# Kernel optimization log

Measured on AMD Instinct MI355X. Metric: run time of the kernel, lower is better.

## Reference

```python
import jax, jax.numpy as jnp
import numpy as np

DIM = 192
SHIFT = 3
PAD = SHIFT // 2  # 1
EPS = 1e-5


def conv1x1(x, w, b):
    # 1x1x1 Conv3d == channel matmul. x: (B,C,D,H,W), w: (O,C), b: (O,)
    return jnp.einsum('bcdhw,oc->bodhw', x, w) + b[None, :, None, None, None]


def group_norm1(x, w, b):
    # GroupNorm(1, C): normalize over (C,D,H,W) per sample, per-channel affine.
    mu = x.mean(axis=(1, 2, 3, 4), keepdims=True)
    var = x.var(axis=(1, 2, 3, 4), keepdims=True)
    xn = (x - mu) * jax.lax.rsqrt(var + EPS)
    return xn * w[None, :, None, None, None] + b[None, :, None, None, None]


def axial_shift(x, axis):
    # reflect-pad all 3 spatial dims, roll channel-chunks along `axis`, crop back.
    R = x.shape[-1]
    xp = jnp.pad(x, ((0, 0), (0, 0), (PAD, PAD), (PAD, PAD), (PAD, PAD)), mode='reflect')
    chunks = jnp.split(xp, SHIFT, axis=1)
    rolled = [jnp.roll(c, s, axis=axis) for c, s in zip(chunks, range(-PAD, PAD + 1))]
    xc = jnp.concatenate(rolled, axis=1)
    return xc[:, :, PAD:PAD + R, PAD:PAD + R, PAD:PAD + R]


def setup_inputs() -> dict:
    key = jax.random.key(0)
    ks = jax.random.split(key, 16)
    B, C, R = 8, DIM, 32
    x = jax.random.normal(ks[0], (B, C, R, R, R), dtype=jnp.float32)
    wmat = lambda k: jax.random.normal(k, (C, C), dtype=jnp.float32) * 0.05
    vec = lambda k: jax.random.normal(k, (C,), dtype=jnp.float32) * 0.05
    return {
        'x': x,
        'w1': wmat(ks[1]), 'b1': vec(ks[2]),
        'n1w': jnp.ones((C,), jnp.float32), 'n1b': jnp.zeros((C,), jnp.float32),
        'w21': wmat(ks[3]), 'b21': vec(ks[4]),
        'w22': wmat(ks[5]), 'b22': vec(ks[6]),
        'w23': wmat(ks[7]), 'b23': vec(ks[8]),
        'n2w': jnp.ones((C,), jnp.float32), 'n2b': jnp.zeros((C,), jnp.float32),
        'w3': wmat(ks[9]), 'b3': vec(ks[10]),
    }


def reference(x, w1, b1, n1w, n1b, w21, b21, w22, b22, w23, b23, n2w, n2b, w3, b3):
    h = conv1x1(x, w1, b1)
    h = group_norm1(h, n1w, n1b)
    h = jax.nn.gelu(h, approximate=False)
    h = axial_shift(h, axis=3)
    h = conv1x1(h, w22, b22)
    h = axial_shift(h, axis=2)
    h = conv1x1(h, w21, b21)
    h = axial_shift(h, axis=4)
    h = conv1x1(h, w23, b23)
    h = jax.nn.gelu(h, approximate=False)
    h = group_norm1(h, n2w, n2b)
    h = conv1x1(h, w3, b3)
    return h
```

## Files before the change

### kernel.cpp

```cpp
#include <hip/hip_runtime.h>
#include <math.h>

#define NCH 192
#define NB 8
#define SPAT 32768
#define TILE_M 64
#define TILES_PER_B (SPAT / TILE_M)
#define NWG (NB * TILES_PER_B)
#define NELEM_PER_B ((size_t)NCH * SPAT)

typedef short s16x8 __attribute__((ext_vector_type(8)));
typedef float f32x4 __attribute__((ext_vector_type(4)));

__device__ __forceinline__ float bf2f(unsigned short h) {
  return __uint_as_float(((unsigned)h) << 16);
}
__device__ __forceinline__ unsigned short f2bf(float f) {
  unsigned u = __float_as_uint(f);
  u += 0x7FFF + ((u >> 16) & 1);
  return (unsigned short)(u >> 16);
}

__device__ __forceinline__ float erf_fast(float x) {
  float ax = fabsf(x);
  float t = 1.0f / fmaf(0.3275911f, ax, 1.0f);
  float p = t * fmaf(t, fmaf(t, fmaf(t, fmaf(t, 1.061405429f, -1.453152027f),
                                     1.421413741f), -0.284496736f), 0.254829592f);
  float r = 1.0f - p * __expf(-ax * ax);
  return copysignf(r, x);
}
__device__ __forceinline__ float gelu_exact(float x) {
  return 0.5f * x * (1.0f + erf_fast(x * 0.70710678118654752f));
}

template <int AX>
__device__ __forceinline__ int shift_src(int p, int s) {
  if (AX == 0) return p;
  const int SH = (AX == 4) ? 0 : (AX == 3) ? 5 : 10;
  int i = (p >> SH) & 31;
  int j = i - s;
  j = (j < 0) ? 1 : j;
  j = (j > 31) ? 30 : j;
  return p + ((j - i) << SH);
}

__device__ __forceinline__ int lds_off(int c, int p, int inner_byte) {
  return (c * 64 + p) * 128 + (inner_byte ^ ((p & 7) << 4));
}

template <int AX, int EPI, int OUTF, int INF, int PERB, int FUSE>
__global__ __launch_bounds__(256, 4)
void gemm_pass(const void* __restrict__ inv,
               const unsigned short* __restrict__ wmat,
               const float* __restrict__ bias,
               void* __restrict__ outv,
               float* __restrict__ partials,
               const float* __restrict__ AC) {
  __shared__ __align__(16) char lds[3 * 64 * 128];
  __shared__ float acs[2 * NCH];
  __shared__ float red[4][2];

  int wg = blockIdx.x;
  int b = wg / TILES_PER_B;
  int p0 = (wg % TILES_PER_B) * TILE_M;
  int tid = threadIdx.x;
  int wave = tid >> 6;
  int lane = tid & 63;
  int col = lane & 15;
  int kg = lane >> 4;

  const unsigned short* wbase = wmat + (PERB ? (size_t)b * NCH * NCH : 0);
  const float* bbase = bias + (PERB ? b * NCH : 0);
  const char* inbytes = (const char*)inv;
  const float* xin = (const float*)inv;

  if (FUSE) {
    for (int i = tid; i < 2 * NCH; i += 256) acs[i] = AC[b * 2 * NCH + i];
    __syncthreads();
  }

  if (INF == 1) {
    int c3 = tid >> 6;
    int p = tid & 63;
    if (c3 < 3) {
      const float* src = xin + (size_t)b * NELEM_PER_B +
                         (size_t)(c3 * 64) * SPAT + (p0 + p);
#pragma unroll
      for (int j = 0; j < 8; ++j) {
        s16x8 v;
#pragma unroll
        for (int u = 0; u < 8; ++u)
          v[u] = (short)f2bf(src[(size_t)(8 * j + u) * SPAT]);
        *(s16x8*)(lds + lds_off(c3, p, j * 16)) = v;
      }
    }
  } else {
#pragma unroll
    for (int j = 0; j < 6; ++j) {
      unsigned g = j * 256 + tid;
      int p = (int)(g / 24u);
      int r24 = (int)(g - 24u * (unsigned)p);
      int c = r24 >> 3;
      int ps = shift_src<AX>(p0 + p, c - 1);
      s16x8 v = *(const s16x8*)(inbytes + ((size_t)b * SPAT + ps) * 384 + r24 * 16);
      if (FUSE) {
        int ch0 = r24 * 8;
#pragma unroll
        for (int u = 0; u < 8; ++u) {
          float f = bf2f((unsigned short)v[u]);
          f = fmaf(f, acs[ch0 + u], acs[NCH + ch0 + u]);
          f = gelu_exact(f);
          v[u] = (short)f2bf(f);
        }
      }
      *(s16x8*)(lds + lds_off(c, p, (r24 & 7) * 16)) = v;
    }
  }
  __syncthreads();

  f32x4 acc[3][4] = {};
#pragma unroll
  for (int ks = 0; ks < 6; ++ks) {
    int k0 = ks * 32 + kg * 8;
    s16x8 af[3];
#pragma unroll
    for (int r = 0; r < 3; ++r) {
      int row = wave * 48 + r * 16 + col;
      af[r] = *(const s16x8*)(wbase + row * NCH + k0);
    }
    int c = k0 >> 6, u = k0 & 63;
    s16x8 bf[4];
#pragma unroll
    for (int m = 0; m < 4; ++m)
      bf[m] = *(const s16x8*)(lds + lds_off(c, m * 16 + col, 2 * u));
#pragma unroll
    for (int r = 0; r < 3; ++r)
#pragma unroll
      for (int m = 0; m < 4; ++m)
        acc[r][m] = __builtin_amdgcn_mfma_f32_16x16x32_bf16(af[r], bf[m], acc[r][m], 0, 0, 0);
  }

  float ssum = 0.f, ssq = 0.f;
  float* outf = (float*)outv;
  if (OUTF == 0) __syncthreads();
#pragma unroll
  for (int r = 0; r < 3; ++r) {
    int rowb = wave * 48 + r * 16 + kg * 4;
    f32x4 bs = *(const f32x4*)(bbase + rowb);
#pragma unroll
    for (int m = 0; m < 4; ++m) {
      int p = m * 16 + col;
      float v[4];
#pragma unroll
      for (int j = 0; j < 4; ++j) {
        float t = acc[r][m][j] + bs[j];
        if (EPI == 2) t = gelu_exact(t);
        if (EPI >= 1) { ssum += t; ssq = fmaf(t, t, ssq); }
        v[j] = t;
      }
      if (OUTF == 0) {
        uint2 pk;
        pk.x = (unsigned)f2bf(v[0]) | ((unsigned)f2bf(v[1]) << 16);
        pk.y = (unsigned)f2bf(v[2]) | ((unsigned)f2bf(v[3]) << 16);
        *(uint2*)(lds + lds_off(rowb >> 6, p, 2 * (rowb & 63))) = pk;
      } else {
#pragma unroll
        for (int j = 0; j < 4; ++j)
          outf[((size_t)b * NCH + rowb + j) * SPAT + p0 + p] = v[j];
      }
    }
  }

  if (OUTF == 0) {
    __syncthreads();
    char* outbytes = (char*)outv + ((size_t)b * SPAT + p0) * 384;
#pragma unroll
    for (int j = 0; j < 6; ++j) {
      unsigned g = j * 256 + tid;
      int p = (int)(g / 24u);
      int r24 = (int)(g - 24u * (unsigned)p);
      int c = r24 >> 3;
      s16x8 v = *(const s16x8*)(lds + lds_off(c, p, (r24 & 7) * 16));
      *(s16x8*)(outbytes + g * 16) = v;
    }
  }

  if (EPI >= 1) {
#pragma unroll
    for (int off = 1; off < 64; off <<= 1) {
      ssum += __shfl_xor(ssum, off, 64);
      ssq += __shfl_xor(ssq, off, 64);
    }
    if (lane == 0) { red[wave][0] = ssum; red[wave][1] = ssq; }
    __syncthreads();
    if (tid == 0) {
      partials[wg * 2]     = red[0][0] + red[1][0] + red[2][0] + red[3][0];
      partials[wg * 2 + 1] = red[0][1] + red[1][1] + red[2][1] + red[3][1];
    }
  }
}

__global__ void stats_finalize(const float* __restrict__ partials,
                               const float* __restrict__ nw,
                               const float* __restrict__ nb,
                               float* __restrict__ AC) {
  int b = blockIdx.x;
  int tid = threadIdx.x;
  __shared__ float s0[256], s1[256];
  float a = 0.f, c = 0.f;
  for (int i = tid; i < TILES_PER_B; i += 256) {
    a += partials[(b * TILES_PER_B + i) * 2];
    c += partials[(b * TILES_PER_B + i) * 2 + 1];
  }
  s0[tid] = a; s1[tid] = c;
  __syncthreads();
  for (int st = 128; st > 0; st >>= 1) {
    if (tid < st) { s0[tid] += s0[tid + st]; s1[tid] += s1[tid + st]; }
    __syncthreads();
  }
  float inv_n = 1.0f / (float)(NELEM_PER_B);
  float mu = s0[0] * inv_n;
  float var = s1[0] * inv_n - mu * mu;
  float rs = rsqrtf(var + 1e-5f);
  if (tid < NCH) {
    float A = rs * nw[tid];
    AC[b * 2 * NCH + tid] = A;
    AC[b * 2 * NCH + NCH + tid] = nb[tid] - mu * A;
  }
}

__global__ void prep_weights(const float* __restrict__ w1, const float* __restrict__ w21,
                             const float* __restrict__ w22, const float* __restrict__ w23,
                             unsigned short* __restrict__ wb) {
  int i = blockIdx.x * 256 + threadIdx.x;
  if (i >= 4 * NCH * NCH) return;
  int m = i / (NCH * NCH), r = i % (NCH * NCH);
  const float* src = (m == 0) ? w1 : (m == 1) ? w22 : (m == 2) ? w21 : w23;
  wb[i] = f2bf(src[r]);
}

__global__ void prep_w3(const float* __restrict__ w3, const float* __restrict__ b3,
                        const float* __restrict__ AC2,
                        unsigned short* __restrict__ w3e, float* __restrict__ b3e) {
  int b = blockIdx.x;
  int o = threadIdx.x;
  if (o >= NCH) return;
  const float* A = AC2 + b * 2 * NCH;
  const float* C = A + NCH;
  float s = b3[o];
  for (int c = 0; c < NCH; ++c) {
    float w = w3[o * NCH + c];
    w3e[((size_t)b * NCH + o) * NCH + c] = f2bf(w * A[c]);
    s = fmaf(w, C[c], s);
  }
  b3e[b * NCH + o] = s;
}

extern "C" void kernel_launch(void* const* d_in, const int* in_sizes, int n_in,
                              void* d_out, int out_size, void* d_ws, size_t ws_size,
                              hipStream_t stream) {
  const float* x   = (const float*)d_in[0];
  const float* w1  = (const float*)d_in[1];
  const float* b1  = (const float*)d_in[2];
  const float* n1w = (const float*)d_in[3];
  const float* n1b = (const float*)d_in[4];
  const float* w21 = (const float*)d_in[5];
  const float* b21 = (const float*)d_in[6];
  const float* w22 = (const float*)d_in[7];
  const float* b22 = (const float*)d_in[8];
  const float* w23 = (const float*)d_in[9];
  const float* b23 = (const float*)d_in[10];
  const float* n2w = (const float*)d_in[11];
  const float* n2b = (const float*)d_in[12];
  const float* w3  = (const float*)d_in[13];
  const float* b3  = (const float*)d_in[14];

  char* ws = (char*)d_ws;
  size_t off = 0;
  unsigned short* wb = (unsigned short*)(ws + off); off += (size_t)4 * NCH * NCH * 2;
  off = (off + 255) & ~(size_t)255;
  unsigned short* w3e = (unsigned short*)(ws + off); off += (size_t)NB * NCH * NCH * 2;
  off = (off + 255) & ~(size_t)255;
  float* b3e = (float*)(ws + off); off += NB * NCH * 4;
  float* AC1 = (float*)(ws + off); off += NB * 2 * NCH * 4;
  float* AC2 = (float*)(ws + off); off += NB * 2 * NCH * 4;
  float* part1 = (float*)(ws + off); off += NWG * 2 * 4;
  float* part2 = (float*)(ws + off); off += NWG * 2 * 4;
  off = (off + 255) & ~(size_t)255;
  unsigned short* R1 = (unsigned short*)(ws + off);
  unsigned short* R2 = (unsigned short*)d_out;

  prep_weights<<<(4 * NCH * NCH + 255) / 256, 256, 0, stream>>>(w1, w21, w22, w23, wb);

  gemm_pass<0, 1, 0, 1, 0, 0><<<NWG, 256, 0, stream>>>(x, wb + 0 * NCH * NCH, b1, R2, part1, nullptr);
  stats_finalize<<<NB, 256, 0, stream>>>(part1, n1w, n1b, AC1);
  gemm_pass<3, 0, 0, 0, 0, 1><<<NWG, 256, 0, stream>>>(R2, wb + 1 * NCH * NCH, b22, R1, nullptr, AC1);
  gemm_pass<2, 0, 0, 0, 0, 0><<<NWG, 256, 0, stream>>>(R1, wb + 2 * NCH * NCH, b21, R2, nullptr, nullptr);
  gemm_pass<4, 2, 0, 0, 0, 0><<<NWG, 256, 0, stream>>>(R2, wb + 3 * NCH * NCH, b23, R1, part2, nullptr);
  stats_finalize<<<NB, 256, 0, stream>>>(part2, n2w, n2b, AC2);
  prep_w3<<<NB, NCH, 0, stream>>>(w3, b3, AC2, w3e, b3e);
  gemm_pass<0, 0, 1, 0, 1, 0><<<NWG, 256, 0, stream>>>(R1, w3e, b3e, d_out, part2, nullptr);
}
```

Measured before the change: 388.4 us.

## Make GEMM passes persistent over 8 tiles with register prefetch and double-buffered LDS

Each workgroup now processes 8 consecutive 64-position tiles instead of one, shrinking the grid to 512 workgroups. The weight fragments are loaded into registers once per workgroup rather than once per tile. The next tile's global loads are issued into registers while the current tile is staged and multiplied, alternating between two LDS buffers. The first pass also reads fp32 input with vector loads, and the LDS swizzle is changed. The costs are higher register pressure (launch bounds lowered to 2 waves per SIMD), double the LDS footprint, and fewer workgroups, which may underfill the GPU.

```diff
diff --git a/kernel.cpp b/kernel.cpp
--- a/kernel.cpp
+++ b/kernel.cpp
@@ -5,8 +5,8 @@
 #define NB 8
 #define SPAT 32768
 #define TILE_M 64
-#define TILES_PER_B (SPAT / TILE_M)
-#define NWG (NB * TILES_PER_B)
+#define TPW 8
+#define NWG_P 512
 #define NELEM_PER_B ((size_t)NCH * SPAT)
 
 typedef short s16x8 __attribute__((ext_vector_type(8)));
@@ -44,25 +44,25 @@
   return p + ((j - i) << SH);
 }
 
-__device__ __forceinline__ int lds_off(int c, int p, int inner_byte) {
-  return (c * 64 + p) * 128 + (inner_byte ^ ((p & 7) << 4));
+__device__ __forceinline__ int lds_off(int c, int p, int u) {
+  return (c * 64 + p) * 128 + 16 * (((u >> 3) ^ (p & 7) ^ (p >> 3)) & 7) + 2 * (u & 7);
 }
 
 template <int AX, int EPI, int OUTF, int INF, int PERB, int FUSE>
-__global__ __launch_bounds__(256, 4)
+__global__ __launch_bounds__(256, 2)
 void gemm_pass(const void* __restrict__ inv,
                const unsigned short* __restrict__ wmat,
                const float* __restrict__ bias,
                void* __restrict__ outv,
                float* __restrict__ partials,
                const float* __restrict__ AC) {
-  __shared__ __align__(16) char lds[3 * 64 * 128];
+  __shared__ __align__(16) char lds[2][3 * 64 * 128];
   __shared__ float acs[2 * NCH];
   __shared__ float red[4][2];
 
   int wg = blockIdx.x;
-  int b = wg / TILES_PER_B;
-  int p0 = (wg % TILES_PER_B) * TILE_M;
+  int b = wg >> 6;
+  int ti0 = (wg & 63) * TPW;
   int tid = threadIdx.x;
   int wave = tid >> 6;
   int lane = tid & 63;
@@ -73,115 +73,150 @@
   const float* bbase = bias + (PERB ? b * NCH : 0);
   const char* inbytes = (const char*)inv;
   const float* xin = (const float*)inv;
-
-  if (FUSE) {
+  float* outf = (float*)outv;
+
+  s16x8 af[6][3];
+#pragma unroll
+  for (int ks = 0; ks < 6; ++ks)
+#pragma unroll
+    for (int r = 0; r < 3; ++r)
+      af[ks][r] = *(const s16x8*)(wbase + (wave * 48 + r * 16 + col) * NCH + ks * 32 + kg * 8);
+
+  if (FUSE)
     for (int i = tid; i < 2 * NCH; i += 256) acs[i] = AC[b * 2 * NCH + i];
+
+  s16x8 vr[6];
+  f32x4 xr[12];
+  {
+    int p0 = ti0 * 64;
+    if (INF == 1) {
+#pragma unroll
+      for (int j = 0; j < 12; ++j) {
+        int q = j * 256 + tid, ch = q >> 4, g = q & 15;
+        xr[j] = *(const f32x4*)(xin + (size_t)b * NELEM_PER_B + (size_t)ch * SPAT + p0 + 4 * g);
+      }
+    } else {
+#pragma unroll
+      for (int j = 0; j < 6; ++j) {
+        unsigned g = j * 256 + tid;
+        int p = (int)(g / 24u), r24 = (int)(g - 24u * (unsigned)p);
+        int ps = shift_src<AX>(p0 + p, (r24 >> 3) - 1);
+        vr[j] = *(const s16x8*)(inbytes + ((size_t)b * SPAT + ps) * 384 + r24 * 16);
+      }
+    }
+  }
+  __syncthreads();
+
+  float ssum = 0.f, ssq = 0.f;
+
+  for (int t = 0; t < TPW; ++t) {
+    char* W = lds[t & 1];
+    int p0 = (ti0 + t) * 64;
+
+    if (INF == 1) {
+#pragma unroll
+      for (int j = 0; j < 12; ++j) {
+        int q = j * 256 + tid, ch = q >> 4, g = q & 15;
+        int c = ch >> 6, u = ch & 63;
+#pragma unroll
+        for (int i = 0; i < 4; ++i)
+          *(unsigned short*)(W + lds_off(c, 4 * g + i, u)) = f2bf(xr[j][i]);
+      }
+    } else {
+#pragma unroll
+      for (int j = 0; j < 6; ++j) {
+        unsigned g = j * 256 + tid;
+        int p = (int)(g / 24u), r24 = (int)(g - 24u * (unsigned)p);
+        s16x8 v = vr[j];
+        if (FUSE) {
+          int ch0 = r24 * 8;
+#pragma unroll
+          for (int u = 0; u < 8; ++u) {
+            float f = bf2f((unsigned short)v[u]);
+            f = fmaf(f, acs[ch0 + u], acs[NCH + ch0 + u]);
+            f = gelu_exact(f);
+            v[u] = (short)f2bf(f);
+          }
+        }
+        *(s16x8*)(W + lds_off(r24 >> 3, p, (r24 & 7) * 8)) = v;
+      }
+    }
+
+    if (t + 1 < TPW) {
+      int p1 = (ti0 + t + 1) * 64;
+      if (INF == 1) {
+#pragma unroll
+        for (int j = 0; j < 12; ++j) {
+          int q = j * 256 + tid, ch = q >> 4, g = q & 15;
+          xr[j] = *(const f32x4*)(xin + (size_t)b * NELEM_PER_B + (size_t)ch * SPAT + p1 + 4 * g);
+        }
+      } else {
+#pragma unroll
+        for (int j = 0; j < 6; ++j) {
+          unsigned g = j * 256 + tid;
+          int p = (int)(g / 24u), r24 = (int)(g - 24u * (unsigned)p);
+          int ps = shift_src<AX>(p1 + p, (r24 >> 3) - 1);
+          vr[j] = *(const s16x8*)(inbytes + ((size_t)b * SPAT + ps) * 384 + r24 * 16);
+        }
+      }
+    }
     __syncthreads();
-  }
-
-  if (INF == 1) {
-    int c3 = tid >> 6;
-    int p = tid & 63;
-    if (c3 < 3) {
-      const float* src = xin + (size_t)b * NELEM_PER_B +
-                         (size_t)(c3 * 64) * SPAT + (p0 + p);
-#pragma unroll
-      for (int j = 0; j < 8; ++j) {
-        s16x8 v;
-#pragma unroll
-        for (int u = 0; u < 8; ++u)
-          v[u] = (short)f2bf(src[(size_t)(8 * j + u) * SPAT]);
-        *(s16x8*)(lds + lds_off(c3, p, j * 16)) = v;
-      }
-    }
-  } else {
-#pragma unroll
-    for (int j = 0; j < 6; ++j) {
-      unsigned g = j * 256 + tid;
-      int p = (int)(g / 24u);
-      int r24 = (int)(g - 24u * (unsigned)p);
-      int c = r24 >> 3;
-      int ps = shift_src<AX>(p0 + p, c - 1);
-      s16x8 v = *(const s16x8*)(inbytes + ((size_t)b * SPAT + ps) * 384 + r24 * 16);
-      if (FUSE) {
-        int ch0 = r24 * 8;
-#pragma unroll
-        for (int u = 0; u < 8; ++u) {
-          float f = bf2f((unsigned short)v[u]);
-          f = fmaf(f, acs[ch0 + u], acs[NCH + ch0 + u]);
-          f = gelu_exact(f);
-          v[u] = (short)f2bf(f);
-        }
-      }
-      *(s16x8*)(lds + lds_off(c, p, (r24 & 7) * 16)) = v;
-    }
-  }
-  __syncthreads();
-
-  f32x4 acc[3][4] = {};
-#pragma unroll
-  for (int ks = 0; ks < 6; ++ks) {
-    int k0 = ks * 32 + kg * 8;
-    s16x8 af[3];
+
+    f32x4 acc[3][4] = {};
+#pragma unroll
+    for (int ks = 0; ks < 6; ++ks) {
+      int k0 = ks * 32 + kg * 8;
+      int c = k0 >> 6, u = k0 & 63;
+      s16x8 bf[4];
+#pragma unroll
+      for (int m = 0; m < 4; ++m)
+        bf[m] = *(const s16x8*)(W + lds_off(c, m * 16 + col, u));
+#pragma unroll
+      for (int r = 0; r < 3; ++r)
+#pragma unroll
+        for (int m = 0; m < 4; ++m)
+          acc[r][m] = __builtin_amdgcn_mfma_f32_16x16x32_bf16(af[ks][r], bf[m], acc[r][m], 0, 0, 0);
+    }
+    __syncthreads();
+
 #pragma unroll
     for (int r = 0; r < 3; ++r) {
-      int row = wave * 48 + r * 16 + col;
-      af[r] = *(const s16x8*)(wbase + row * NCH + k0);
-    }
-    int c = k0 >> 6, u = k0 & 63;
-    s16x8 bf[4];
-#pragma unroll
-    for (int m = 0; m < 4; ++m)
-      bf[m] = *(const s16x8*)(lds + lds_off(c, m * 16 + col, 2 * u));
-#pragma unroll
-    for (int r = 0; r < 3; ++r)
-#pragma unroll
-      for (int m = 0; m < 4; ++m)
-        acc[r][m] = __builtin_amdgcn_mfma_f32_16x16x32_bf16(af[r], bf[m], acc[r][m], 0, 0, 0);
-  }
-
-  float ssum = 0.f, ssq = 0.f;
-  float* outf = (float*)outv;
-  if (OUTF == 0) __syncthreads();
-#pragma unroll
-  for (int r = 0; r < 3; ++r) {
-    int rowb = wave * 48 + r * 16 + kg * 4;
-    f32x4 bs = *(const f32x4*)(bbase + rowb);
-#pragma unroll
-    for (int m = 0; m < 4; ++m) {
-      int p = m * 16 + col;
-      float v[4];
-#pragma unroll
-      for (int j = 0; j < 4; ++j) {
-        float t = acc[r][m][j] + bs[j];
-        if (EPI == 2) t = gelu_exact(t);
-        if (EPI >= 1) { ssum += t; ssq = fmaf(t, t, ssq); }
-        v[j] = t;
-      }
-      if (OUTF == 0) {
-        uint2 pk;
-        pk.x = (unsigned)f2bf(v[0]) | ((unsigned)f2bf(v[1]) << 16);
-        pk.y = (unsigned)f2bf(v[2]) | ((unsigned)f2bf(v[3]) << 16);
-        *(uint2*)(lds + lds_off(rowb >> 6, p, 2 * (rowb & 63))) = pk;
-      } else {
-#pragma unroll
-        for (int j = 0; j < 4; ++j)
-          outf[((size_t)b * NCH + rowb + j) * SPAT + p0 + p] = v[j];
-      }
-    }
-  }
-
-  if (OUTF == 0) {
-    __syncthreads();
-    char* outbytes = (char*)outv + ((size_t)b * SPAT + p0) * 384;
-#pragma unroll
-    for (int j = 0; j < 6; ++j) {
-      unsigned g = j * 256 + tid;
-      int p = (int)(g / 24u);
-      int r24 = (int)(g - 24u * (unsigned)p);
-      int c = r24 >> 3;
-      s16x8 v = *(const s16x8*)(lds + lds_off(c, p, (r24 & 7) * 16));
-      *(s16x8*)(outbytes + g * 16) = v;
+      int rowb = wave * 48 + r * 16 + kg * 4;
+      f32x4 bs = *(const f32x4*)(bbase + rowb);
+#pragma unroll
+      for (int m = 0; m < 4; ++m) {
+        int p = m * 16 + col;
+        float v[4];
+#pragma unroll
+        for (int j = 0; j < 4; ++j) {
+          float tv = acc[r][m][j] + bs[j];
+          if (EPI == 2) tv = gelu_exact(tv);
+          if (EPI >= 1) { ssum += tv; ssq = fmaf(tv, tv, ssq); }
+          v[j] = tv;
+        }
+        if (OUTF == 0) {
+          uint2 pk;
+          pk.x = (unsigned)f2bf(v[0]) | ((unsigned)f2bf(v[1]) << 16);
+          pk.y = (unsigned)f2bf(v[2]) | ((unsigned)f2bf(v[3]) << 16);
+          *(uint2*)(W + lds_off(rowb >> 6, p, rowb & 63)) = pk;
+        } else {
+#pragma unroll
+          for (int j = 0; j < 4; ++j)
+            outf[((size_t)b * NCH + rowb + j) * SPAT + p0 + p] = v[j];
+        }
+      }
+    }
+
+    if (OUTF == 0) {
+      __syncthreads();
+      char* outbytes = (char*)outv + ((size_t)b * SPAT + p0) * 384;
+#pragma unroll
+      for (int j = 0; j < 6; ++j) {
+        unsigned g = j * 256 + tid;
+        int p = (int)(g / 24u), r24 = (int)(g - 24u * (unsigned)p);
+        s16x8 v = *(const s16x8*)(W + lds_off(r24 >> 3, p, (r24 & 7) * 8));
+        *(s16x8*)(outbytes + g * 16) = v;
+      }
     }
   }
 
@@ -208,9 +243,9 @@
   int tid = threadIdx.x;
   __shared__ float s0[256], s1[256];
   float a = 0.f, c = 0.f;
-  for (int i = tid; i < TILES_PER_B; i += 256) {
-    a += partials[(b * TILES_PER_B + i) * 2];
-    c += partials[(b * TILES_PER_B + i) * 2 + 1];
+  for (int i = tid; i < 64; i += 256) {
+    a += partials[(b * 64 + i) * 2];
+    c += partials[(b * 64 + i) * 2 + 1];
   }
   s0[tid] = a; s1[tid] = c;
   __syncthreads();
@@ -284,20 +319,20 @@
   float* b3e = (float*)(ws + off); off += NB * NCH * 4;
   float* AC1 = (float*)(ws + off); off += NB * 2 * NCH * 4;
   float* AC2 = (float*)(ws + off); off += NB * 2 * NCH * 4;
-  float* part1 = (float*)(ws + off); off += NWG * 2 * 4;
-  float* part2 = (float*)(ws + off); off += NWG * 2 * 4;
+  float* part1 = (float*)(ws + off); off += NWG_P * 2 * 4;
+  float* part2 = (float*)(ws + off); off += NWG_P * 2 * 4;
   off = (off + 255) & ~(size_t)255;
   unsigned short* R1 = (unsigned short*)(ws + off);
   unsigned short* R2 = (unsigned short*)d_out;
 
   prep_weights<<<(4 * NCH * NCH + 255) / 256, 256, 0, stream>>>(w1, w21, w22, w23, wb);
 
-  gemm_pass<0, 1, 0, 1, 0, 0><<<NWG, 256, 0, stream>>>(x, wb + 0 * NCH * NCH, b1, R2, part1, nullptr);
+  gemm_pass<0, 1, 0, 1, 0, 0><<<NWG_P, 256, 0, stream>>>(x, wb + 0 * NCH * NCH, b1, R2, part1, nullptr);
   stats_finalize<<<NB, 256, 0, stream>>>(part1, n1w, n1b, AC1);
-  gemm_pass<3, 0, 0, 0, 0, 1><<<NWG, 256, 0, stream>>>(R2, wb + 1 * NCH * NCH, b22, R1, nullptr, AC1);
-  gemm_pass<2, 0, 0, 0, 0, 0><<<NWG, 256, 0, stream>>>(R1, wb + 2 * NCH * NCH, b21, R2, nullptr, nullptr);
-  gemm_pass<4, 2, 0, 0, 0, 0><<<NWG, 256, 0, stream>>>(R2, wb + 3 * NCH * NCH, b23, R1, part2, nullptr);
+  gemm_pass<3, 0, 0, 0, 0, 1><<<NWG_P, 256, 0, stream>>>(R2, wb + 1 * NCH * NCH, b22, R1, nullptr, AC1);
+  gemm_pass<2, 0, 0, 0, 0, 0><<<NWG_P, 256, 0, stream>>>(R1, wb + 2 * NCH * NCH, b21, R2, nullptr, nullptr);
+  gemm_pass<4, 2, 0, 0, 0, 0><<<NWG_P, 256, 0, stream>>>(R2, wb + 3 * NCH * NCH, b23, R1, part2, nullptr);
   stats_finalize<<<NB, 256, 0, stream>>>(part2, n2w, n2b, AC2);
   prep_w3<<<NB, NCH, 0, stream>>>(w3, b3, AC2, w3e, b3e);
-  gemm_pass<0, 0, 1, 0, 1, 0><<<NWG, 256, 0, stream>>>(R1, w3e, b3e, d_out, part2, nullptr);
-}
+  gemm_pass<0, 0, 1, 0, 1, 0><<<NWG_P, 256, 0, stream>>>(R1, w3e, b3e, d_out, part2, nullptr);
+}
```

Result: slower. 504.8 us (+30.0%).
